# Kernel optimization log

Hardware: AMD Instinct MI355X
Metric: run time of the kernel (lower is better)

The kernel has to match this reference:

```python
import jax, jax.numpy as jnp
import numpy as np

N_ENT = 10000
MM_DIM = 768
ST_DIM = 256
COMPS = 5
TAU = 0.1
TOPK = 6
BN_EPS = 1e-5


def _normalize(x):
    # matches neibor_mnce's local normalize: x / (||x|| + 1e-12)
    return x / (jnp.linalg.norm(x, axis=-1, keepdims=True) + 1e-12)


def _neibor_mnce(stru, mm):
    # stru: [N, d], mm: [N, d]
    sn = _normalize(stru)
    mn = _normalize(mm)
    sm = jnp.exp((sn @ mn.T) / TAU)          # [N, N] exp(cossim/tau)
    max_sm_idx = jnp.argmax(sm, axis=-1)     # [N]
    rows = mn[max_sm_idx] @ mn.T             # [N, N] = mm_distMap[max_sm_idx]
    _, top_idx = jax.lax.top_k(rows, TOPK)   # [N, TOPK]
    pos = jnp.take_along_axis(sm, top_idx, axis=-1)  # [N, TOPK]
    return jnp.mean(-jnp.log(pos.sum(axis=-1) / sm.sum(axis=-1)))


def setup_inputs() -> dict:
    key = jax.random.key(0)
    ks = jax.random.split(key, 6)
    st_feats = jax.random.normal(ks[0], (N_ENT, ST_DIM, COMPS), dtype=jnp.float32)
    mm_feats = jax.random.normal(ks[1], (N_ENT, MM_DIM), dtype=jnp.float32)
    # 5 stacked encoders (t,r,i,j,k): Linear(mm->st), GELU, Linear(st->st), BatchNorm1d
    W1 = jax.random.normal(ks[2], (COMPS, ST_DIM, MM_DIM), dtype=jnp.float32) * np.float32(np.sqrt(2.0 / MM_DIM))
    b1 = jnp.zeros((COMPS, ST_DIM), dtype=jnp.float32)
    W2 = jax.random.normal(ks[3], (COMPS, ST_DIM, ST_DIM), dtype=jnp.float32) * np.float32(np.sqrt(2.0 / ST_DIM))
    b2 = jnp.zeros((COMPS, ST_DIM), dtype=jnp.float32)
    gamma = jnp.ones((COMPS, ST_DIM), dtype=jnp.float32)
    beta = jnp.zeros((COMPS, ST_DIM), dtype=jnp.float32)
    return {"st_feats": st_feats, "mm_feats": mm_feats,
            "W1": W1, "b1": b1, "W2": W2, "b2": b2,
            "gamma": gamma, "beta": beta}


def reference(st_feats, mm_feats, W1, b1, W2, b2, gamma, beta):
    # Encode mm_feats through the 5 parallel MLP+BN encoders (vectorized over comp axis e)
    h = jnp.einsum('nd,eod->neo', mm_feats, W1) + b1          # [N, 5, st]
    h = jax.nn.gelu(h, approximate=False)
    h = jnp.einsum('nek,eok->neo', h, W2) + b2                # [N, 5, st]
    # BatchNorm1d in training mode: batch stats over N, biased variance
    mu = h.mean(axis=0)
    var = h.var(axis=0)
    mm_enc = (h - mu) / jnp.sqrt(var + BN_EPS) * gamma + beta  # [N, 5, st]

    # rand_ratio = 1 -> seq_cands is all True, full set used
    losses = []
    for c in range(COMPS):
        losses.append(_neibor_mnce(st_feats[:, :, c], mm_enc[:, c, :]))
    loss = sum(losses) / jnp.float32(COMPS)

    # torch.stack([t,r,i,j,k], dim=-1) -> [N, st_dim, 5]
    mm_out = jnp.transpose(mm_enc, (0, 2, 1))
    return (mm_out, loss)
```

## Files before the change

kernel.cpp:

```cpp
#include <hip/hip_runtime.h>
#include <hip/hip_bf16.h>
#include <math.h>

#define N_ENT 10000
#define NPAD 10112
#define NCT 79
#define CS1 8
#define CS2 4
#define INV_TAU 10.0f

typedef __attribute__((ext_vector_type(8))) short bf16x8;
typedef __attribute__((ext_vector_type(4))) float f32x4;

__device__ __forceinline__ bool better(float v, int i, float bv, int bi) {
    return (v > bv) || (v == bv && i < bi);
}

__device__ __forceinline__ float sel6f(const float (&a)[6], int k) {
    return k == 0 ? a[0] : k == 1 ? a[1] : k == 2 ? a[2] : k == 3 ? a[3] : k == 4 ? a[4] : a[5];
}
__device__ __forceinline__ int sel6i(const int (&a)[6], int k) {
    return k == 0 ? a[0] : k == 1 ? a[1] : k == 2 ? a[2] : k == 3 ? a[3] : k == 4 ? a[4] : a[5];
}

__device__ __forceinline__ void topk_insert(float (&v)[6], int (&ix)[6], float nv, int ni) {
    if (!better(nv, ni, v[5], ix[5])) return;
    bool b0 = better(v[0], ix[0], nv, ni);
    bool b1 = better(v[1], ix[1], nv, ni);
    bool b2 = better(v[2], ix[2], nv, ni);
    bool b3 = better(v[3], ix[3], nv, ni);
    bool b4 = better(v[4], ix[4], nv, ni);
    float o0 = v[0], o1 = v[1], o2 = v[2], o3 = v[3], o4 = v[4];
    int j0 = ix[0], j1 = ix[1], j2 = ix[2], j3 = ix[3], j4 = ix[4];
    v[0] = b0 ? o0 : nv;              ix[0] = b0 ? j0 : ni;
    v[1] = b1 ? o1 : (b0 ? nv : o0);  ix[1] = b1 ? j1 : (b0 ? ni : j0);
    v[2] = b2 ? o2 : (b1 ? nv : o1);  ix[2] = b2 ? j2 : (b1 ? ni : j1);
    v[3] = b3 ? o3 : (b2 ? nv : o2);  ix[3] = b3 ? j3 : (b2 ? ni : j2);
    v[4] = b4 ? o4 : (b3 ? nv : o3);  ix[4] = b4 ? j4 : (b3 ? ni : j3);
    v[5] = b4 ? nv : o4;              ix[5] = b4 ? ni : j4;
}

__device__ __forceinline__ ushort f2bf(float x) {
    __hip_bfloat16 h = __float2bfloat16(x);
    return *(ushort*)&h;
}

template <bool GELU>
__global__ __launch_bounds__(256) void enc_gemm(const float* __restrict__ A, size_t Astride,
                                                const float* __restrict__ B,
                                                const float* __restrict__ bias,
                                                float* __restrict__ C, int M, int K) {
    const int e = blockIdx.z;
    const float* Ae = A + (size_t)e * Astride;
    const float* Be = B + (size_t)e * 256 * K;
    const float* be = bias + e * 256;
    float* Ce = C + (size_t)e * (size_t)M * 256;
    const int n0 = blockIdx.x * 64;
    const int o0 = blockIdx.y * 64;
    __shared__ float As[16][64];
    __shared__ float Bs[16][64];
    const int tid = threadIdx.x;
    const int tx = tid & 15, ty = tid >> 4;
    const int li = tid >> 2;
    const int lk = (tid & 3) * 4;
    float acc[4][4];
#pragma unroll
    for (int i = 0; i < 4; i++)
#pragma unroll
        for (int j = 0; j < 4; j++) acc[i][j] = 0.f;
    for (int kc = 0; kc < K; kc += 16) {
        float4 av = make_float4(0.f, 0.f, 0.f, 0.f);
        if (n0 + li < M) av = *(const float4*)(Ae + (size_t)(n0 + li) * K + kc + lk);
        As[lk + 0][li] = av.x; As[lk + 1][li] = av.y; As[lk + 2][li] = av.z; As[lk + 3][li] = av.w;
        float4 bv = *(const float4*)(Be + (size_t)(o0 + li) * K + kc + lk);
        Bs[lk + 0][li] = bv.x; Bs[lk + 1][li] = bv.y; Bs[lk + 2][li] = bv.z; Bs[lk + 3][li] = bv.w;
        __syncthreads();
#pragma unroll
        for (int k = 0; k < 16; k++) {
            float4 a4 = *(const float4*)&As[k][ty * 4];
            float4 b4 = *(const float4*)&Bs[k][tx * 4];
            float a[4] = {a4.x, a4.y, a4.z, a4.w}, b[4] = {b4.x, b4.y, b4.z, b4.w};
#pragma unroll
            for (int i = 0; i < 4; i++)
#pragma unroll
                for (int j = 0; j < 4; j++) acc[i][j] = fmaf(a[i], b[j], acc[i][j]);
        }
        __syncthreads();
    }
#pragma unroll
    for (int i = 0; i < 4; i++) {
        int gr = n0 + ty * 4 + i;
        if (gr >= M) continue;
#pragma unroll
        for (int j = 0; j < 4; j++) {
            int go = o0 + tx * 4 + j;
            float v = acc[i][j] + be[go];
            if (GELU) v = 0.5f * v * (1.0f + erff(v * 0.70710678118654752f));
            Ce[(size_t)gr * 256 + go] = v;
        }
    }
}

__global__ __launch_bounds__(256) void bn_stats(const float* __restrict__ E,
                                                const float* __restrict__ gamma,
                                                const float* __restrict__ beta,
                                                float* __restrict__ bn_a, float* __restrict__ bn_b) {
    const int ch = blockIdx.x;
    const int e = ch >> 8, o = ch & 255;
    const float* p = E + (size_t)e * N_ENT * 256 + o;
    float s = 0.f, ss = 0.f;
    for (int n = threadIdx.x; n < N_ENT; n += 256) {
        float v = p[(size_t)n * 256];
        s += v; ss += v * v;
    }
    __shared__ float sh1[4], sh2[4];
    int lane = threadIdx.x & 63, w = threadIdx.x >> 6;
    for (int off = 32; off; off >>= 1) { s += __shfl_down(s, off); ss += __shfl_down(ss, off); }
    if (lane == 0) { sh1[w] = s; sh2[w] = ss; }
    __syncthreads();
    if (threadIdx.x == 0) {
        s = sh1[0] + sh1[1] + sh1[2] + sh1[3];
        ss = sh2[0] + sh2[1] + sh2[2] + sh2[3];
        float mu = s * (1.f / N_ENT);
        float var = ss * (1.f / N_ENT) - mu * mu;
        float r = rsqrtf(var + 1e-5f);
        float a = gamma[ch] * r;
        bn_a[ch] = a;
        bn_b[ch] = beta[ch] - mu * a;
    }
}

__global__ __launch_bounds__(256) void bn_apply(float* __restrict__ E,
                                                const float* __restrict__ bn_a,
                                                const float* __restrict__ bn_b,
                                                float* __restrict__ out) {
    size_t idx = (size_t)blockIdx.x * 256 + threadIdx.x;
    int e = (int)(idx / ((size_t)N_ENT * 256));
    size_t rem = idx - (size_t)e * N_ENT * 256;
    int n = (int)(rem >> 8), o = (int)(rem & 255);
    int ch = (e << 8) | o;
    float v = E[idx] * bn_a[ch] + bn_b[ch];
    E[idx] = v;
    out[(size_t)n * 1280 + o * 5 + e] = v;
}

__global__ __launch_bounds__(256) void rownorm(const float* __restrict__ base, size_t rowstride,
                                               int elemstride, float* __restrict__ rn) {
    int n = blockIdx.x;
    float v = base[(size_t)n * rowstride + (size_t)threadIdx.x * elemstride];
    float s = v * v;
    __shared__ float sh[4];
    int lane = threadIdx.x & 63, w = threadIdx.x >> 6;
    for (int off = 32; off; off >>= 1) s += __shfl_down(s, off);
    if (lane == 0) sh[w] = s;
    __syncthreads();
    if (threadIdx.x == 0) {
        s = sh[0] + sh[1] + sh[2] + sh[3];
        rn[n] = 1.f / (sqrtf(s) + 1e-12f);
    }
}

__global__ __launch_bounds__(256) void build_snb(const float* __restrict__ st, int c,
                                                 const float* __restrict__ rns,
                                                 ushort* __restrict__ snb) {
    int n = blockIdx.x, o = threadIdx.x;
    float v = 0.f;
    if (n < N_ENT) v = st[(size_t)n * 1280 + o * 5 + c] * rns[n];
    snb[(size_t)n * 256 + o] = f2bf(v);
}

__global__ __launch_bounds__(256) void build_mnb(const float* __restrict__ E, int c,
                                                 const float* __restrict__ rnm,
                                                 ushort* __restrict__ mnb, float* __restrict__ mn) {
    int n = blockIdx.x, o = threadIdx.x;
    float v = 0.f;
    if (n < N_ENT) {
        v = E[((size_t)c * N_ENT + n) * 256 + o] * rnm[n];
        mn[(size_t)n * 256 + o] = v;
    }
    mnb[(size_t)n * 256 + o] = f2bf(v);
}

__global__ __launch_bounds__(256, 2) void pass1_mfma(const ushort* __restrict__ snb,
                                                     const ushort* __restrict__ mnb,
                                                     float* __restrict__ pmax, int* __restrict__ pidx,
                                                     float* __restrict__ psum) {
    __shared__ ushort Bs[128][72];
    const int bx = blockIdx.x;
    const int cs = blockIdx.y;
    const int tid = threadIdx.x;
    const int w = tid >> 6, lane = tid & 63;
    const int lr = lane & 15;
    const int lg = lane >> 4;
    const int rbase = bx * 128 + w * 32;

    bf16x8 a[2][8];
#pragma unroll
    for (int rf = 0; rf < 2; rf++)
#pragma unroll
        for (int ks = 0; ks < 8; ks++)
            a[rf][ks] = *(const bf16x8*)(snb + (size_t)(rbase + rf * 16 + lr) * 256 + ks * 32 + lg * 8);

    float sume[2][4], maxv[2][4];
    int maxi[2][4];
#pragma unroll
    for (int rf = 0; rf < 2; rf++)
#pragma unroll
        for (int r = 0; r < 4; r++) { sume[rf][r] = 0.f; maxv[rf][r] = -1e30f; maxi[rf][r] = 0x7fffffff; }

    const int srow = tid >> 1;
    const int sp = (tid & 1) * 32;

    for (int ct = cs; ct < NCT; ct += CS1) {
        const int c0 = ct * 128;
        f32x4 acc[2][8];
#pragma unroll
        for (int rf = 0; rf < 2; rf++)
#pragma unroll
            for (int fj = 0; fj < 8; fj++) acc[rf][fj] = (f32x4)(0.f);
        for (int kc = 0; kc < 4; kc++) {
            const ushort* gsrc = mnb + (size_t)(c0 + srow) * 256 + kc * 64 + sp;
            float4 g0 = *(const float4*)(gsrc);
            float4 g1 = *(const float4*)(gsrc + 8);
            float4 g2 = *(const float4*)(gsrc + 16);
            float4 g3 = *(const float4*)(gsrc + 24);
            __syncthreads();
            *(float4*)&Bs[srow][sp + 0] = g0;
            *(float4*)&Bs[srow][sp + 8] = g1;
            *(float4*)&Bs[srow][sp + 16] = g2;
            *(float4*)&Bs[srow][sp + 24] = g3;
            __syncthreads();
#pragma unroll
            for (int ki = 0; ki < 2; ki++) {
                const int ks = kc * 2 + ki;
#pragma unroll
                for (int fj = 0; fj < 8; fj++) {
                    bf16x8 b = *(const bf16x8*)&Bs[fj * 16 + lr][ki * 32 + lg * 8];
                    acc[0][fj] = __builtin_amdgcn_mfma_f32_16x16x32_bf16(a[0][ks], b, acc[0][fj], 0, 0, 0);
                    acc[1][fj] = __builtin_amdgcn_mfma_f32_16x16x32_bf16(a[1][ks], b, acc[1][fj], 0, 0, 0);
                }
            }
        }
#pragma unroll
        for (int fj = 0; fj < 8; fj++) {
            int col = c0 + fj * 16 + lr;
            bool ok = col < N_ENT;
#pragma unroll
            for (int rf = 0; rf < 2; rf++)
#pragma unroll
                for (int r = 0; r < 4; r++) {
                    float v = acc[rf][fj][r];
                    if (ok) {
                        sume[rf][r] += __expf(v * INV_TAU);
                        if (v > maxv[rf][r]) { maxv[rf][r] = v; maxi[rf][r] = col; }
                    }
                }
        }
    }
#pragma unroll
    for (int m = 1; m < 16; m <<= 1) {
#pragma unroll
        for (int rf = 0; rf < 2; rf++)
#pragma unroll
            for (int r = 0; r < 4; r++) {
                float ov = __shfl_xor(maxv[rf][r], m);
                int oi = __shfl_xor(maxi[rf][r], m);
                float os = __shfl_xor(sume[rf][r], m);
                sume[rf][r] += os;
                if (better(ov, oi, maxv[rf][r], maxi[rf][r])) { maxv[rf][r] = ov; maxi[rf][r] = oi; }
            }
    }
    if (lr == 0) {
#pragma unroll
        for (int rf = 0; rf < 2; rf++)
#pragma unroll
            for (int r = 0; r < 4; r++) {
                int gr = rbase + rf * 16 + 4 * lg + r;
                if (gr < N_ENT) {
                    pmax[(size_t)cs * N_ENT + gr] = maxv[rf][r];
                    pidx[(size_t)cs * N_ENT + gr] = maxi[rf][r];
                    psum[(size_t)cs * N_ENT + gr] = sume[rf][r];
                }
            }
    }
}

__global__ __launch_bounds__(256) void p1_combine(const float* __restrict__ pmax,
                                                  const int* __restrict__ pidx,
                                                  const float* __restrict__ psum,
                                                  int* __restrict__ amax, float* __restrict__ denom) {
    int n = blockIdx.x * 256 + threadIdx.x;
    if (n >= N_ENT) return;
    float bm = -1e30f; int bi = 0x7fffffff; float s = 0.f;
    for (int cs = 0; cs < CS1; cs++) {
        float v = pmax[(size_t)cs * N_ENT + n];
        int ii = pidx[(size_t)cs * N_ENT + n];
        s += psum[(size_t)cs * N_ENT + n];
        if (v > bm || (v == bm && ii < bi)) { bm = v; bi = ii; }
    }
    amax[n] = bi;
    denom[n] = s;
}

__global__ __launch_bounds__(256, 2) void pass2_mfma(const ushort* __restrict__ mnb,
                                                     const int* __restrict__ amax,
                                                     float* __restrict__ tval, int* __restrict__ tidx) {
    __shared__ ushort Bs[128][72];
    __shared__ int rowsel[64];
    const int bx = blockIdx.x;
    const int cs = blockIdx.y;
    const int tid = threadIdx.x;
    const int w = tid >> 6, lane = tid & 63;
    const int lr = lane & 15;
    const int lg = lane >> 4;
    const int rbase = bx * 64 + w * 16;
    if (tid < 64) {
        int g = bx * 64 + tid;
        rowsel[tid] = (g < N_ENT) ? amax[g] : 0;
    }
    __syncthreads();

    bf16x8 a[8];
    {
        int src = rowsel[w * 16 + lr];
#pragma unroll
        for (int ks = 0; ks < 8; ks++)
            a[ks] = *(const bf16x8*)(mnb + (size_t)src * 256 + ks * 32 + lg * 8);
    }
    float tv[4][6]; int ti[4][6];
#pragma unroll
    for (int r = 0; r < 4; r++)
#pragma unroll
        for (int s = 0; s < 6; s++) { tv[r][s] = -1e30f; ti[r][s] = 0x7fffffff; }

    const int srow = tid >> 1;
    const int sp = (tid & 1) * 32;

    for (int ct = cs; ct < NCT; ct += CS2) {
        const int c0 = ct * 128;
        f32x4 acc[8];
#pragma unroll
        for (int fj = 0; fj < 8; fj++) acc[fj] = (f32x4)(0.f);
        for (int kc = 0; kc < 4; kc++) {
            const ushort* gsrc = mnb + (size_t)(c0 + srow) * 256 + kc * 64 + sp;
            float4 g0 = *(const float4*)(gsrc);
            float4 g1 = *(const float4*)(gsrc + 8);
            float4 g2 = *(const float4*)(gsrc + 16);
            float4 g3 = *(const float4*)(gsrc + 24);
            __syncthreads();
            *(float4*)&Bs[srow][sp + 0] = g0;
            *(float4*)&Bs[srow][sp + 8] = g1;
            *(float4*)&Bs[srow][sp + 16] = g2;
            *(float4*)&Bs[srow][sp + 24] = g3;
            __syncthreads();
#pragma unroll
            for (int ki = 0; ki < 2; ki++) {
                const int ks = kc * 2 + ki;
#pragma unroll
                for (int fj = 0; fj < 8; fj++) {
                    bf16x8 b = *(const bf16x8*)&Bs[fj * 16 + lr][ki * 32 + lg * 8];
                    acc[fj] = __builtin_amdgcn_mfma_f32_16x16x32_bf16(a[ks], b, acc[fj], 0, 0, 0);
                }
            }
        }
#pragma unroll
        for (int fj = 0; fj < 8; fj++) {
            int col = c0 + fj * 16 + lr;
            if (col < N_ENT) {
#pragma unroll
                for (int r = 0; r < 4; r++) topk_insert(tv[r], ti[r], acc[fj][r], col);
            }
        }
    }
#pragma unroll
    for (int r = 0; r < 4; r++) {
        int gr = rbase + 4 * lg + r;
        int used = 0;
#pragma unroll
        for (int s = 0; s < 6; s++) {
            float hv = sel6f(tv[r], used);
            int hi = sel6i(ti[r], used);
            float bv = hv; int bi = hi;
#pragma unroll
            for (int m = 1; m < 16; m <<= 1) {
                float ov = __shfl_xor(bv, m);
                int oi = __shfl_xor(bi, m);
                if (better(ov, oi, bv, bi)) { bv = ov; bi = oi; }
            }
            if (hi == bi) used++;
            if (lr == 0 && gr < N_ENT) {
                tval[((size_t)cs * N_ENT + gr) * 6 + s] = bv;
                tidx[((size_t)cs * N_ENT + gr) * 6 + s] = bi;
            }
        }
    }
}

__global__ __launch_bounds__(64) void p2_combine(const float* __restrict__ tval,
                                                 const int* __restrict__ tidx,
                                                 const float* __restrict__ denom,
                                                 const float* __restrict__ st, int c,
                                                 const float* __restrict__ rns,
                                                 const float* __restrict__ mn,
                                                 float* __restrict__ lsum) {
    const int n = blockIdx.x;
    __shared__ float sv[24];
    __shared__ int sidx[24];
    __shared__ int sel[6];
    int t = threadIdx.x;
    if (t < 24) {
        int cs = t / 6, s = t % 6;
        sv[t] = tval[((size_t)cs * N_ENT + n) * 6 + s];
        sidx[t] = tidx[((size_t)cs * N_ENT + n) * 6 + s];
    }
    __syncthreads();
    if (t == 0) {
        float pv = 1e30f; int pi = -1;
        for (int s = 0; s < 6; s++) {
            float bv = -1e30f; int bi = 0x7fffffff;
            for (int u = 0; u < 24; u++) {
                float v = sv[u]; int i = sidx[u];
                if (better(pv, pi, v, i) && better(v, i, bv, bi)) { bv = v; bi = i; }
            }
            sel[s] = bi;
            pv = bv; pi = bi;
        }
    }
    __syncthreads();
    float pos = 0.f;
    for (int s = 0; s < 6; s++) {
        const float* mr = mn + (size_t)sel[s] * 256;
        float d = 0.f;
        for (int dd = t; dd < 256; dd += 64)
            d += st[(size_t)n * 1280 + (size_t)dd * 5 + c] * mr[dd];
        for (int off = 32; off; off >>= 1) d += __shfl_down(d, off);
        if (t == 0) pos += __expf(d * rns[n] * INV_TAU);
    }
    if (t == 0) {
        float l = logf(denom[n]) - logf(pos);
        atomicAdd(lsum, l);
    }
}

__global__ void init_lsum(float* lsum) { lsum[0] = 0.f; }

__global__ void finalize_loss(const float* __restrict__ lsum, float* __restrict__ out) {
    out[12800000] = lsum[0] * (1.f / (N_ENT * 5.0f));
}

extern "C" void kernel_launch(void* const* d_in, const int* in_sizes, int n_in,
                              void* d_out, int out_size, void* d_ws, size_t ws_size,
                              hipStream_t stream) {
    (void)in_sizes; (void)n_in; (void)out_size; (void)ws_size;
    const float* st = (const float*)d_in[0];
    const float* mm = (const float*)d_in[1];
    const float* W1 = (const float*)d_in[2];
    const float* b1 = (const float*)d_in[3];
    const float* W2 = (const float*)d_in[4];
    const float* b2 = (const float*)d_in[5];
    const float* gamma = (const float*)d_in[6];
    const float* beta = (const float*)d_in[7];
    float* out = (float*)d_out;

    float* bufH = (float*)d_ws;
    float* bufE = bufH + 12800000ull;
    float* fp = bufE + 12800000ull;
    float* bn_a = fp; fp += 1280;
    float* bn_b = fp; fp += 1280;
    float* rns = fp; fp += N_ENT;
    float* rnm = fp; fp += N_ENT;
    float* denom = fp; fp += N_ENT;
    float* pmax = fp; fp += CS1 * N_ENT;
    float* psum = fp; fp += CS1 * N_ENT;
    float* tval = fp; fp += CS2 * N_ENT * 6;
    float* lsum = fp; fp += 8;
    int* ip = (int*)fp;
    int* amax = ip; ip += N_ENT;
    int* pidx = ip; ip += CS1 * N_ENT;
    int* tidx = ip; ip += CS2 * N_ENT * 6;
    float* mn = bufH;
    ushort* snb = (ushort*)(bufH + 2560000);
    ushort* mnb = snb + (size_t)NPAD * 256;

    init_lsum<<<1, 1, 0, stream>>>(lsum);

    dim3 gg(157, 4, 5);
    enc_gemm<true><<<gg, 256, 0, stream>>>(mm, 0, W1, b1, bufH, N_ENT, 768);
    enc_gemm<false><<<gg, 256, 0, stream>>>(bufH, (size_t)N_ENT * 256, W2, b2, bufE, N_ENT, 256);

    bn_stats<<<1280, 256, 0, stream>>>(bufE, gamma, beta, bn_a, bn_b);
    bn_apply<<<50000, 256, 0, stream>>>(bufE, bn_a, bn_b, out);

    for (int c = 0; c < 5; c++) {
        rownorm<<<N_ENT, 256, 0, stream>>>(st + c, 1280, 5, rns);
        rownorm<<<N_ENT, 256, 0, stream>>>(bufE + (size_t)c * N_ENT * 256, 256, 1, rnm);
        build_snb<<<NPAD, 256, 0, stream>>>(st, c, rns, snb);
        build_mnb<<<NPAD, 256, 0, stream>>>(bufE, c, rnm, mnb, mn);
        pass1_mfma<<<dim3(NPAD / 128, CS1), 256, 0, stream>>>(snb, mnb, pmax, pidx, psum);
        p1_combine<<<40, 256, 0, stream>>>(pmax, pidx, psum, amax, denom);
        pass2_mfma<<<dim3(NPAD / 64, CS2), 256, 0, stream>>>(mnb, amax, tval, tidx);
        p2_combine<<<N_ENT, 64, 0, stream>>>(tval, tidx, denom, st, c, rns, mn, lsum);
    }
    finalize_loss<<<1, 1, 0, stream>>>(lsum, out);
}
```

Before: 3.444 ms.

## Move encoder GEMMs to split-bf16 MFMA and prefetch pass tiles

```diff
diff --git a/kernel.cpp b/kernel.cpp
--- a/kernel.cpp
+++ b/kernel.cpp
@@ -5,8 +5,8 @@
 #define N_ENT 10000
 #define NPAD 10112
 #define NCT 79
-#define CS1 8
-#define CS2 4
+#define CS1 13
+#define CS2 13
 #define INV_TAU 10.0f
 
 typedef __attribute__((ext_vector_type(8))) short bf16x8;
@@ -44,90 +44,154 @@
     __hip_bfloat16 h = __float2bfloat16(x);
     return *(ushort*)&h;
 }
+__device__ __forceinline__ float bf2f(ushort h) {
+    unsigned int u = ((unsigned int)h) << 16;
+    return __uint_as_float(u);
+}
+
+__global__ __launch_bounds__(256) void conv_w(const float* __restrict__ w, ushort* __restrict__ hi,
+                                              ushort* __restrict__ lo, int n) {
+    int i = blockIdx.x * 256 + threadIdx.x;
+    if (i >= n) return;
+    float v = w[i];
+    ushort h = f2bf(v);
+    hi[i] = h;
+    lo[i] = f2bf(v - bf2f(h));
+}
 
 template <bool GELU>
-__global__ __launch_bounds__(256) void enc_gemm(const float* __restrict__ A, size_t Astride,
-                                                const float* __restrict__ B,
-                                                const float* __restrict__ bias,
-                                                float* __restrict__ C, int M, int K) {
+__global__ __launch_bounds__(256, 2) void enc_mfma(const float* __restrict__ A, size_t Astride, int K,
+                                                   const ushort* __restrict__ Whi,
+                                                   const ushort* __restrict__ Wlo,
+                                                   const float* __restrict__ bias,
+                                                   float* __restrict__ C) {
+    __shared__ ushort Ah[128][40], Al[128][40], Bh[128][40], Bl[128][40];
     const int e = blockIdx.z;
     const float* Ae = A + (size_t)e * Astride;
-    const float* Be = B + (size_t)e * 256 * K;
+    const ushort* Whe = Whi + (size_t)e * 256 * K;
+    const ushort* Wle = Wlo + (size_t)e * 256 * K;
     const float* be = bias + e * 256;
-    float* Ce = C + (size_t)e * (size_t)M * 256;
-    const int n0 = blockIdx.x * 64;
-    const int o0 = blockIdx.y * 64;
-    __shared__ float As[16][64];
-    __shared__ float Bs[16][64];
+    float* Ce = C + (size_t)e * N_ENT * 256;
+    const int n0 = blockIdx.x * 128;
+    const int o0 = blockIdx.y * 128;
     const int tid = threadIdx.x;
-    const int tx = tid & 15, ty = tid >> 4;
-    const int li = tid >> 2;
-    const int lk = (tid & 3) * 4;
-    float acc[4][4];
-#pragma unroll
-    for (int i = 0; i < 4; i++)
-#pragma unroll
-        for (int j = 0; j < 4; j++) acc[i][j] = 0.f;
-    for (int kc = 0; kc < K; kc += 16) {
-        float4 av = make_float4(0.f, 0.f, 0.f, 0.f);
-        if (n0 + li < M) av = *(const float4*)(Ae + (size_t)(n0 + li) * K + kc + lk);
-        As[lk + 0][li] = av.x; As[lk + 1][li] = av.y; As[lk + 2][li] = av.z; As[lk + 3][li] = av.w;
-        float4 bv = *(const float4*)(Be + (size_t)(o0 + li) * K + kc + lk);
-        Bs[lk + 0][li] = bv.x; Bs[lk + 1][li] = bv.y; Bs[lk + 2][li] = bv.z; Bs[lk + 3][li] = bv.w;
+    const int w = tid >> 6, lane = tid & 63;
+    const int lr = lane & 15, lg = lane >> 4;
+    const int srow = tid >> 1;
+    const int skf = (tid & 1) * 16;
+
+    f32x4 acc[2][8];
+#pragma unroll
+    for (int rf = 0; rf < 2; rf++)
+#pragma unroll
+        for (int fj = 0; fj < 8; fj++) acc[rf][fj] = (f32x4)(0.f);
+
+    const int nkc = K >> 5;
+    float4 ga[4];
+    uint4 gwh[2], gwl[2];
+    const bool rowok = (n0 + srow) < N_ENT;
+
+#define ENC_ISSUE(KC)                                                                  \
+    {                                                                                  \
+        const float* ap = Ae + (size_t)(n0 + srow) * K + (KC) * 32 + skf;              \
+        if (rowok) {                                                                   \
+            ga[0] = *(const float4*)(ap + 0);  ga[1] = *(const float4*)(ap + 4);       \
+            ga[2] = *(const float4*)(ap + 8);  ga[3] = *(const float4*)(ap + 12);      \
+        } else {                                                                       \
+            ga[0] = ga[1] = ga[2] = ga[3] = make_float4(0.f, 0.f, 0.f, 0.f);           \
+        }                                                                              \
+        const ushort* hp = Whe + (size_t)(o0 + srow) * K + (KC) * 32 + skf;            \
+        gwh[0] = *(const uint4*)(hp); gwh[1] = *(const uint4*)(hp + 8);                \
+        const ushort* lp = Wle + (size_t)(o0 + srow) * K + (KC) * 32 + skf;            \
+        gwl[0] = *(const uint4*)(lp); gwl[1] = *(const uint4*)(lp + 8);                \
+    }
+
+    ENC_ISSUE(0)
+    for (int kc = 0; kc < nkc; kc++) {
         __syncthreads();
 #pragma unroll
-        for (int k = 0; k < 16; k++) {
-            float4 a4 = *(const float4*)&As[k][ty * 4];
-            float4 b4 = *(const float4*)&Bs[k][tx * 4];
-            float a[4] = {a4.x, a4.y, a4.z, a4.w}, b[4] = {b4.x, b4.y, b4.z, b4.w};
-#pragma unroll
-            for (int i = 0; i < 4; i++)
-#pragma unroll
-                for (int j = 0; j < 4; j++) acc[i][j] = fmaf(a[i], b[j], acc[i][j]);
-        }
+        for (int j = 0; j < 4; j++) {
+            float4 v = ga[j];
+            ushort h0 = f2bf(v.x), h1 = f2bf(v.y), h2 = f2bf(v.z), h3 = f2bf(v.w);
+            ushort l0 = f2bf(v.x - bf2f(h0)), l1 = f2bf(v.y - bf2f(h1));
+            ushort l2 = f2bf(v.z - bf2f(h2)), l3 = f2bf(v.w - bf2f(h3));
+            *(ushort4*)&Ah[srow][skf + j * 4] = make_ushort4(h0, h1, h2, h3);
+            *(ushort4*)&Al[srow][skf + j * 4] = make_ushort4(l0, l1, l2, l3);
+        }
+        *(uint4*)&Bh[srow][skf] = gwh[0];
+        *(uint4*)&Bh[srow][skf + 8] = gwh[1];
+        *(uint4*)&Bl[srow][skf] = gwl[0];
+        *(uint4*)&Bl[srow][skf + 8] = gwl[1];
         __syncthreads();
-    }
-#pragma unroll
-    for (int i = 0; i < 4; i++) {
-        int gr = n0 + ty * 4 + i;
-        if (gr >= M) continue;
-#pragma unroll
-        for (int j = 0; j < 4; j++) {
-            int go = o0 + tx * 4 + j;
-            float v = acc[i][j] + be[go];
-            if (GELU) v = 0.5f * v * (1.0f + erff(v * 0.70710678118654752f));
-            Ce[(size_t)gr * 256 + go] = v;
-        }
-    }
-}
-
-__global__ __launch_bounds__(256) void bn_stats(const float* __restrict__ E,
-                                                const float* __restrict__ gamma,
-                                                const float* __restrict__ beta,
-                                                float* __restrict__ bn_a, float* __restrict__ bn_b) {
-    const int ch = blockIdx.x;
-    const int e = ch >> 8, o = ch & 255;
-    const float* p = E + (size_t)e * N_ENT * 256 + o;
+        if (kc + 1 < nkc) ENC_ISSUE(kc + 1)
+        bf16x8 ah[2], al[2];
+#pragma unroll
+        for (int rf = 0; rf < 2; rf++) {
+            ah[rf] = *(const bf16x8*)&Ah[w * 32 + rf * 16 + lr][lg * 8];
+            al[rf] = *(const bf16x8*)&Al[w * 32 + rf * 16 + lr][lg * 8];
+        }
+#pragma unroll
+        for (int fj = 0; fj < 8; fj++) {
+            bf16x8 bh = *(const bf16x8*)&Bh[fj * 16 + lr][lg * 8];
+            bf16x8 bl = *(const bf16x8*)&Bl[fj * 16 + lr][lg * 8];
+#pragma unroll
+            for (int rf = 0; rf < 2; rf++) {
+                acc[rf][fj] = __builtin_amdgcn_mfma_f32_16x16x32_bf16(ah[rf], bh, acc[rf][fj], 0, 0, 0);
+                acc[rf][fj] = __builtin_amdgcn_mfma_f32_16x16x32_bf16(ah[rf], bl, acc[rf][fj], 0, 0, 0);
+                acc[rf][fj] = __builtin_amdgcn_mfma_f32_16x16x32_bf16(al[rf], bh, acc[rf][fj], 0, 0, 0);
+            }
+        }
+    }
+#undef ENC_ISSUE
+#pragma unroll
+    for (int rf = 0; rf < 2; rf++) {
+#pragma unroll
+        for (int r = 0; r < 4; r++) {
+            int gr = n0 + w * 32 + rf * 16 + 4 * lg + r;
+            if (gr >= N_ENT) continue;
+#pragma unroll
+            for (int fj = 0; fj < 8; fj++) {
+                int go = o0 + fj * 16 + lr;
+                float v = acc[rf][fj][r] + be[go];
+                if (GELU) v = 0.5f * v * (1.0f + erff(v * 0.70710678118654752f));
+                Ce[(size_t)gr * 256 + go] = v;
+            }
+        }
+    }
+}
+
+__global__ __launch_bounds__(256) void bn_part(const float* __restrict__ E,
+                                               float* __restrict__ ps, float* __restrict__ pss) {
+    const int e = blockIdx.x, chunk = blockIdx.y;
+    const float* base = E + ((size_t)e * N_ENT + (size_t)chunk * 250) * 256;
+    const int o = threadIdx.x;
     float s = 0.f, ss = 0.f;
-    for (int n = threadIdx.x; n < N_ENT; n += 256) {
-        float v = p[(size_t)n * 256];
+    for (int r = 0; r < 250; r++) {
+        float v = base[(size_t)r * 256 + o];
         s += v; ss += v * v;
     }
-    __shared__ float sh1[4], sh2[4];
-    int lane = threadIdx.x & 63, w = threadIdx.x >> 6;
-    for (int off = 32; off; off >>= 1) { s += __shfl_down(s, off); ss += __shfl_down(ss, off); }
-    if (lane == 0) { sh1[w] = s; sh2[w] = ss; }
-    __syncthreads();
-    if (threadIdx.x == 0) {
-        s = sh1[0] + sh1[1] + sh1[2] + sh1[3];
-        ss = sh2[0] + sh2[1] + sh2[2] + sh2[3];
-        float mu = s * (1.f / N_ENT);
-        float var = ss * (1.f / N_ENT) - mu * mu;
-        float r = rsqrtf(var + 1e-5f);
-        float a = gamma[ch] * r;
-        bn_a[ch] = a;
-        bn_b[ch] = beta[ch] - mu * a;
-    }
+    ps[((size_t)e * 40 + chunk) * 256 + o] = s;
+    pss[((size_t)e * 40 + chunk) * 256 + o] = ss;
+}
+
+__global__ __launch_bounds__(256) void bn_finish(const float* __restrict__ ps,
+                                                 const float* __restrict__ pss,
+                                                 const float* __restrict__ gamma,
+                                                 const float* __restrict__ beta,
+                                                 float* __restrict__ bn_a, float* __restrict__ bn_b) {
+    const int e = blockIdx.x, o = threadIdx.x;
+    float s = 0.f, ss = 0.f;
+    for (int c = 0; c < 40; c++) {
+        s += ps[((size_t)e * 40 + c) * 256 + o];
+        ss += pss[((size_t)e * 40 + c) * 256 + o];
+    }
+    float mu = s * (1.f / N_ENT);
+    float var = ss * (1.f / N_ENT) - mu * mu;
+    float r = rsqrtf(var + 1e-5f);
+    int ch = e * 256 + o;
+    float a = gamma[ch] * r;
+    bn_a[ch] = a;
+    bn_b[ch] = beta[ch] - mu * a;
 }
 
 __global__ __launch_bounds__(256) void bn_apply(float* __restrict__ E,
@@ -181,6 +245,13 @@
     mnb[(size_t)n * 256 + o] = f2bf(v);
 }
 
+#define P_ISSUE(CT, KC)                                                                  \
+    {                                                                                    \
+        const ushort* gsrc = mnb + (size_t)((CT) * 128 + srow) * 256 + (KC) * 64 + sp;   \
+        g0 = *(const float4*)(gsrc);       g1 = *(const float4*)(gsrc + 8);              \
+        g2 = *(const float4*)(gsrc + 16);  g3 = *(const float4*)(gsrc + 24);             \
+    }
+
 __global__ __launch_bounds__(256, 2) void pass1_mfma(const ushort* __restrict__ snb,
                                                      const ushort* __restrict__ mnb,
                                                      float* __restrict__ pmax, int* __restrict__ pidx,
@@ -210,7 +281,9 @@
 
     const int srow = tid >> 1;
     const int sp = (tid & 1) * 32;
-
+    float4 g0, g1, g2, g3;
+
+    P_ISSUE(cs, 0)
     for (int ct = cs; ct < NCT; ct += CS1) {
         const int c0 = ct * 128;
         f32x4 acc[2][8];
@@ -219,17 +292,17 @@
 #pragma unroll
             for (int fj = 0; fj < 8; fj++) acc[rf][fj] = (f32x4)(0.f);
         for (int kc = 0; kc < 4; kc++) {
-            const ushort* gsrc = mnb + (size_t)(c0 + srow) * 256 + kc * 64 + sp;
-            float4 g0 = *(const float4*)(gsrc);
-            float4 g1 = *(const float4*)(gsrc + 8);
-            float4 g2 = *(const float4*)(gsrc + 16);
-            float4 g3 = *(const float4*)(gsrc + 24);
             __syncthreads();
             *(float4*)&Bs[srow][sp + 0] = g0;
             *(float4*)&Bs[srow][sp + 8] = g1;
             *(float4*)&Bs[srow][sp + 16] = g2;
             *(float4*)&Bs[srow][sp + 24] = g3;
             __syncthreads();
+            {
+                int nct = ct, nkc = kc + 1;
+                if (nkc == 4) { nkc = 0; nct = ct + CS1; }
+                if (nct < NCT) P_ISSUE(nct, nkc)
+            }
 #pragma unroll
             for (int ki = 0; ki < 2; ki++) {
                 const int ks = kc * 2 + ki;
@@ -335,24 +408,26 @@
 
     const int srow = tid >> 1;
     const int sp = (tid & 1) * 32;
-
+    float4 g0, g1, g2, g3;
+
+    P_ISSUE(cs, 0)
     for (int ct = cs; ct < NCT; ct += CS2) {
         const int c0 = ct * 128;
         f32x4 acc[8];
 #pragma unroll
         for (int fj = 0; fj < 8; fj++) acc[fj] = (f32x4)(0.f);
         for (int kc = 0; kc < 4; kc++) {
-            const ushort* gsrc = mnb + (size_t)(c0 + srow) * 256 + kc * 64 + sp;
-            float4 g0 = *(const float4*)(gsrc);
-            float4 g1 = *(const float4*)(gsrc + 8);
-            float4 g2 = *(const float4*)(gsrc + 16);
-            float4 g3 = *(const float4*)(gsrc + 24);
             __syncthreads();
             *(float4*)&Bs[srow][sp + 0] = g0;
             *(float4*)&Bs[srow][sp + 8] = g1;
             *(float4*)&Bs[srow][sp + 16] = g2;
             *(float4*)&Bs[srow][sp + 24] = g3;
             __syncthreads();
+            {
+                int nct = ct, nkc = kc + 1;
+                if (nkc == 4) { nkc = 0; nct = ct + CS2; }
+                if (nct < NCT) P_ISSUE(nct, nkc)
+            }
 #pragma unroll
             for (int ki = 0; ki < 2; ki++) {
                 const int ks = kc * 2 + ki;
@@ -399,26 +474,25 @@
 __global__ __launch_bounds__(64) void p2_combine(const float* __restrict__ tval,
                                                  const int* __restrict__ tidx,
                                                  const float* __restrict__ denom,
-                                                 const float* __restrict__ st, int c,
-                                                 const float* __restrict__ rns,
+                                                 const ushort* __restrict__ snb,
                                                  const float* __restrict__ mn,
                                                  float* __restrict__ lsum) {
     const int n = blockIdx.x;
-    __shared__ float sv[24];
-    __shared__ int sidx[24];
+    __shared__ float sv[CS2 * 6];
+    __shared__ int sidx[CS2 * 6];
     __shared__ int sel[6];
     int t = threadIdx.x;
-    if (t < 24) {
-        int cs = t / 6, s = t % 6;
-        sv[t] = tval[((size_t)cs * N_ENT + n) * 6 + s];
-        sidx[t] = tidx[((size_t)cs * N_ENT + n) * 6 + s];
+    for (int u = t; u < CS2 * 6; u += 64) {
+        int cs = u / 6, s = u % 6;
+        sv[u] = tval[((size_t)cs * N_ENT + n) * 6 + s];
+        sidx[u] = tidx[((size_t)cs * N_ENT + n) * 6 + s];
     }
     __syncthreads();
     if (t == 0) {
         float pv = 1e30f; int pi = -1;
         for (int s = 0; s < 6; s++) {
             float bv = -1e30f; int bi = 0x7fffffff;
-            for (int u = 0; u < 24; u++) {
+            for (int u = 0; u < CS2 * 6; u++) {
                 float v = sv[u]; int i = sidx[u];
                 if (better(pv, pi, v, i) && better(v, i, bv, bi)) { bv = v; bi = i; }
             }
@@ -432,9 +506,9 @@
         const float* mr = mn + (size_t)sel[s] * 256;
         float d = 0.f;
         for (int dd = t; dd < 256; dd += 64)
-            d += st[(size_t)n * 1280 + (size_t)dd * 5 + c] * mr[dd];
+            d += bf2f(snb[(size_t)n * 256 + dd]) * mr[dd];
         for (int off = 32; off; off >>= 1) d += __shfl_down(d, off);
-        if (t == 0) pos += __expf(d * rns[n] * INV_TAU);
+        if (t == 0) pos += __expf(d * INV_TAU);
     }
     if (t == 0) {
         float l = logf(denom[n]) - logf(pos);
@@ -465,6 +539,13 @@
     float* bufH = (float*)d_ws;
     float* bufE = bufH + 12800000ull;
     float* fp = bufE + 12800000ull;
+    ushort* w1hi = (ushort*)fp;
+    ushort* w1lo = w1hi + 983040;
+    ushort* w2hi = w1lo + 983040;
+    ushort* w2lo = w2hi + 327680;
+    fp += (2 * 983040 + 2 * 327680 + 2) / 2;
+    float* ps = fp; fp += 5 * 40 * 256;
+    float* pss = fp; fp += 5 * 40 * 256;
     float* bn_a = fp; fp += 1280;
     float* bn_b = fp; fp += 1280;
     float* rns = fp; fp += N_ENT;
@@ -483,12 +564,14 @@
     ushort* mnb = snb + (size_t)NPAD * 256;
 
     init_lsum<<<1, 1, 0, stream>>>(lsum);
-
-    dim3 gg(157, 4, 5);
-    enc_gemm<true><<<gg, 256, 0, stream>>>(mm, 0, W1, b1, bufH, N_ENT, 768);
-    enc_gemm<false><<<gg, 256, 0, stream>>>(bufH, (size_t)N_ENT * 256, W2, b2, bufE, N_ENT, 256);
-
-    bn_stats<<<1280, 256, 0, stream>>>(bufE, gamma, beta, bn_a, bn_b);
+    conv_w<<<3840, 256, 0, stream>>>(W1, w1hi, w1lo, 983040);
+    conv_w<<<1280, 256, 0, stream>>>(W2, w2hi, w2lo, 327680);
+
+    enc_mfma<true><<<dim3(79, 2, 5), 256, 0, stream>>>(mm, 0, 768, w1hi, w1lo, b1, bufH);
+    enc_mfma<false><<<dim3(79, 2, 5), 256, 0, stream>>>(bufH, (size_t)N_ENT * 256, 256, w2hi, w2lo, b2, bufE);
+
+    bn_part<<<dim3(5, 40), 256, 0, stream>>>(bufE, ps, pss);
+    bn_finish<<<5, 256, 0, stream>>>(ps, pss, gamma, beta, bn_a, bn_b);
     bn_apply<<<50000, 256, 0, stream>>>(bufE, bn_a, bn_b, out);
 
     for (int c = 0; c < 5; c++) {
@@ -499,7 +582,7 @@
         pass1_mfma<<<dim3(NPAD / 128, CS1), 256, 0, stream>>>(snb, mnb, pmax, pidx, psum);
         p1_combine<<<40, 256, 0, stream>>>(pmax, pidx, psum, amax, denom);
         pass2_mfma<<<dim3(NPAD / 64, CS2), 256, 0, stream>>>(mnb, amax, tval, tidx);
-        p2_combine<<<N_ENT, 64, 0, stream>>>(tval, tidx, denom, st, c, rns, mn, lsum);
+        p2_combine<<<N_ENT, 64, 0, stream>>>(tval, tidx, denom, snb, mn, lsum);
     }
     finalize_loss<<<1, 1, 0, stream>>>(lsum, out);
 }
```

Measured after the change: 3.400 ms. Within noise of the previous version (-1.3%).
